# Kernel optimization log

Measured on AMD Instinct MI355X. Metric: run time of the kernel, lower is better.

The kernel has to match this reference:

```python
import jax, jax.numpy as jnp
import numpy as np

N_NODES = 100000
N_EDGES = 1600000
IN_CH = 128
HID = 32
N_GRAPHS = 64


def _gcn_conv(x, src, dst, W, b, n_nodes):
    # PyG GCNConv defaults: x' = D^{-1/2} (A + I) D^{-1/2} (x W) + b
    h = x @ W                                   # [N, out]
    loop = jnp.arange(n_nodes, dtype=src.dtype)
    s = jnp.concatenate([src, loop])            # add self-loops
    d = jnp.concatenate([dst, loop])
    deg = jax.ops.segment_sum(jnp.ones_like(d, dtype=h.dtype), d, num_segments=n_nodes)
    dinv = jnp.where(deg > 0, jax.lax.rsqrt(deg), 0.0)
    norm = dinv[s] * dinv[d]                    # [E+N]
    msg = h[s] * norm[:, None]                  # gather + scale
    out = jax.ops.segment_sum(msg, d, num_segments=n_nodes)  # scatter-add
    return out + b


def setup_inputs() -> dict:
    key = jax.random.key(0)
    ks = jax.random.split(key, 8)
    x = jax.random.normal(ks[0], (N_NODES, IN_CH), dtype=jnp.float32)
    edge_index = jax.random.randint(ks[1], (2, N_EDGES), 0, N_NODES, dtype=jnp.int32)
    batch = jnp.sort(jax.random.randint(ks[2], (N_NODES,), 0, N_GRAPHS, dtype=jnp.int32))
    W1 = jax.random.normal(ks[3], (IN_CH, HID), dtype=jnp.float32) * (1.0 / np.sqrt(IN_CH))
    b1 = jnp.zeros((HID,), dtype=jnp.float32)
    W2 = jax.random.normal(ks[4], (HID, HID), dtype=jnp.float32) * (1.0 / np.sqrt(HID))
    b2 = jnp.zeros((HID,), dtype=jnp.float32)
    Ws = jax.random.normal(ks[5], (HID, HID), dtype=jnp.float32) * (1.0 / np.sqrt(HID))
    bs = jnp.zeros((HID,), dtype=jnp.float32)
    return {"x": x, "edge_index": edge_index, "batch": batch,
            "W1": W1, "b1": b1, "W2": W2, "b2": b2, "Ws": Ws, "bs": bs}


def reference(x, edge_index, batch, W1, b1, W2, b2, Ws, bs):
    src, dst = edge_index[0], edge_index[1]
    n = x.shape[0]
    h = _gcn_conv(x, src, dst, W1, b1, n)
    h = jax.nn.relu(h)
    h = _gcn_conv(h, src, dst, W2, b2, n)       # [N, HID] node embeddings
    # global_mean_pool over graph ids
    ones = jnp.ones((n,), dtype=h.dtype)
    cnt = jax.ops.segment_sum(ones, batch, num_segments=N_GRAPHS)
    gsum = jax.ops.segment_sum(h, batch, num_segments=N_GRAPHS)
    g = gsum / jnp.maximum(cnt, 1.0)[:, None]   # [G, HID]
    summary = g @ Ws + bs
    return summary, h
```

## Files before the change

kernel.cpp:

```cpp
#include <hip/hip_runtime.h>

#define N_NODES  100000
#define N_EDGES  1600000
#define IN_CH    128
#define HID      32
#define N_GRAPHS 64

#define NBIN   391
#define CHUNK  4096
#define MGRID  391
#define STG    5120

#define OFF_B      0
#define OFF_EDGEPK 3200000
#define OFF_CSR    4800000
#define OFF_COLT   6400000
#define OFF_BINB   6400391
#define OFF_ROWPTR 6400784
#define OFF_DINV   6500785

__device__ __forceinline__ unsigned bfr(float f) {
    unsigned u = __float_as_uint(f);
    u += 0x7fffu + ((u >> 16) & 1u);
    return u >> 16;
}
__device__ __forceinline__ float bflo(unsigned w) { return __uint_as_float(w << 16); }
__device__ __forceinline__ float bfhi(unsigned w) { return __uint_as_float(w & 0xffff0000u); }

__global__ __launch_bounds__(512) void hist_kernel(const int* __restrict__ dst,
                                                   int* __restrict__ H) {
    __shared__ int s[512];
    int t = threadIdx.x, wg = blockIdx.x;
    s[t] = 0;
    __syncthreads();
    int e0 = wg * CHUNK, e1 = min(e0 + CHUNK, N_EDGES);
    for (int e = e0 + t; e < e1; e += 512) {
        int d = dst[e];
        if ((unsigned)d < N_NODES) atomicAdd(&s[d >> 8], 1);
    }
    __syncthreads();
    if (t < NBIN) H[t * MGRID + wg] = s[t];
}

__global__ __launch_bounds__(512) void scanrow_kernel(int* __restrict__ H,
                                                      int* __restrict__ colT) {
    __shared__ int s[512];
    int t = threadIdx.x, bin = blockIdx.x;
    s[t] = (t < MGRID) ? H[bin * MGRID + t] : 0;
    __syncthreads();
    for (int off = 1; off < 512; off <<= 1) {
        int v = (t >= off) ? s[t - off] : 0;
        __syncthreads();
        if (t >= off) s[t] += v;
        __syncthreads();
    }
    if (t < MGRID) H[bin * MGRID + t] = t ? s[t - 1] : 0;
    if (t == 0) colT[bin] = s[MGRID - 1];
}

__global__ __launch_bounds__(512) void scanbase_kernel(const int* __restrict__ colT,
                                                       int* __restrict__ binB,
                                                       int* __restrict__ row_ptr) {
    __shared__ int s[512];
    int t = threadIdx.x;
    s[t] = (t < NBIN) ? colT[t] : 0;
    __syncthreads();
    for (int off = 1; off < 512; off <<= 1) {
        int v = (t >= off) ? s[t - off] : 0;
        __syncthreads();
        if (t >= off) s[t] += v;
        __syncthreads();
    }
    if (t < NBIN) binB[t] = t ? s[t - 1] : 0;
    if (t == 0) { binB[NBIN] = s[NBIN - 1]; row_ptr[N_NODES] = s[NBIN - 1]; }
}

__global__ __launch_bounds__(512) void msplit_kernel(const int* __restrict__ src,
                                                     const int* __restrict__ dst,
                                                     const int* __restrict__ H,
                                                     const int* __restrict__ binB,
                                                     int* __restrict__ edgepk) {
    __shared__ int s[512];
    __shared__ int cur[NBIN];
    __shared__ int gb[NBIN];
    __shared__ int stage[CHUNK];
    __shared__ int gof[CHUNK];
    int t = threadIdx.x, wg = blockIdx.x;
    s[t] = 0;
    __syncthreads();
    int e0 = wg * CHUNK, e1 = min(e0 + CHUNK, N_EDGES);
    for (int e = e0 + t; e < e1; e += 512) {
        int d = dst[e];
        if ((unsigned)d < N_NODES) atomicAdd(&s[d >> 8], 1);
    }
    __syncthreads();
    for (int off = 1; off < 512; off <<= 1) {
        int v = (t >= off) ? s[t - off] : 0;
        __syncthreads();
        if (t >= off) s[t] += v;
        __syncthreads();
    }
    if (t < NBIN) {
        int lo = t ? s[t - 1] : 0;
        cur[t] = lo;
        gb[t] = binB[t] + H[t * MGRID + wg] - lo;
    }
    __syncthreads();
    for (int e = e0 + t; e < e1; e += 512) {
        int d = dst[e];
        if ((unsigned)d < N_NODES) {
            int b = d >> 8;
            int p = atomicAdd(&cur[b], 1);
            stage[p] = (src[e] << 8) | (d & 255);
            gof[p] = gb[b];
        }
    }
    __syncthreads();
    int total = s[511];
    for (int p = t; p < total; p += 512)
        edgepk[gof[p] + p] = stage[p];
}

__global__ __launch_bounds__(256) void csr2_kernel(const int* __restrict__ edgepk,
                                                   const int* __restrict__ binB,
                                                   int* __restrict__ row_ptr,
                                                   float* __restrict__ dinv,
                                                   int* __restrict__ csr) {
    __shared__ int cnt[256], s[256], cur[256];
    __shared__ int stage[STG];
    int t = threadIdx.x, bin = blockIdx.x;
    int ebase = binB[bin], eend = binB[bin + 1];
    int n = eend - ebase;
    cnt[t] = 0;
    __syncthreads();
    for (int p = ebase + t; p < eend; p += 256)
        atomicAdd(&cnt[edgepk[p] & 255], 1);
    __syncthreads();
    s[t] = cnt[t];
    __syncthreads();
    for (int off = 1; off < 256; off <<= 1) {
        int v = (t >= off) ? s[t - off] : 0;
        __syncthreads();
        if (t >= off) s[t] += v;
        __syncthreads();
    }
    int excl = t ? s[t - 1] : 0;
    int node = (bin << 8) + t;
    if (node < N_NODES) {
        dinv[node] = rsqrtf((float)(cnt[t] + 1));
        row_ptr[node] = ebase + excl;
    }
    cur[t] = excl;
    __syncthreads();
    for (int p = ebase + t; p < eend; p += 256) {
        int w = edgepk[p];
        int l = atomicAdd(&cur[w & 255], 1);
        int sv = w >> 8;
        if (l < STG) stage[l] = sv;
        else csr[ebase + l] = sv;
    }
    __syncthreads();
    int lim = min(n, STG);
    for (int l = t; l < lim; l += 256)
        csr[ebase + l] = stage[l];
}

#define XS1 132
__global__ __launch_bounds__(256) void gemm1_kernel(const float* __restrict__ x,
                                                    const float* __restrict__ W1,
                                                    const float* __restrict__ dinv,
                                                    unsigned* __restrict__ Bu) {
    __shared__ float Wl[IN_CH * HID];
    __shared__ float xs[32 * XS1];
    int tid = threadIdx.x;
    for (int j = tid; j < IN_CH * HID / 4; j += 256)
        ((float4*)Wl)[j] = ((const float4*)W1)[j];
    int row0 = blockIdx.x * 32;
    const float4* x4 = (const float4*)(x + (size_t)row0 * IN_CH);
    for (int j = tid; j < 32 * IN_CH / 4; j += 256) {
        int r = j >> 5, k4 = j & 31;
        ((float4*)&xs[r * XS1])[k4] = x4[j];
    }
    __syncthreads();
    int r = tid >> 3, cg = (tid & 7) * 4;
    const float* xr = &xs[r * XS1];
    float4 acc = {0.f, 0.f, 0.f, 0.f};
    #pragma unroll 8
    for (int k = 0; k < IN_CH; ++k) {
        float xv = xr[k];
        float4 w = *(const float4*)&Wl[k * HID + cg];
        acc.x += xv * w.x; acc.y += xv * w.y; acc.z += xv * w.z; acc.w += xv * w.w;
    }
    int row = row0 + r;
    float dv = dinv[row];
    uint2 p;
    p.x = bfr(acc.x * dv) | (bfr(acc.y * dv) << 16);
    p.y = bfr(acc.z * dv) | (bfr(acc.w * dv) << 16);
    *(uint2*)&Bu[(size_t)row * 16 + (tid & 7) * 2] = p;
}

#define XS2 36
__global__ __launch_bounds__(256) void gemm2_kernel(const float* __restrict__ in,
                                                    const float* __restrict__ W2,
                                                    const float* __restrict__ dinv,
                                                    unsigned* __restrict__ Bu) {
    __shared__ float Wl[HID * HID];
    __shared__ float xs[32 * XS2];
    int tid = threadIdx.x;
    ((float4*)Wl)[tid] = ((const float4*)W2)[tid];
    int row0 = blockIdx.x * 32;
    const float4* in4 = (const float4*)(in + (size_t)row0 * HID);
    {
        int r = tid >> 3, k4 = tid & 7;
        ((float4*)&xs[r * XS2])[k4] = in4[tid];
    }
    __syncthreads();
    int r = tid >> 3, cg = (tid & 7) * 4;
    const float* xr = &xs[r * XS2];
    float4 acc = {0.f, 0.f, 0.f, 0.f};
    #pragma unroll
    for (int k = 0; k < HID; ++k) {
        float xv = xr[k];
        float4 w = *(const float4*)&Wl[k * HID + cg];
        acc.x += xv * w.x; acc.y += xv * w.y; acc.z += xv * w.z; acc.w += xv * w.w;
    }
    int row = row0 + r;
    float dv = dinv[row];
    uint2 p;
    p.x = bfr(acc.x * dv) | (bfr(acc.y * dv) << 16);
    p.y = bfr(acc.z * dv) | (bfr(acc.w * dv) << 16);
    *(uint2*)&Bu[(size_t)row * 16 + (tid & 7) * 2] = p;
}

__global__ __launch_bounds__(256) void layer_kernel(const unsigned* __restrict__ Bu,
                                                    const int* __restrict__ csr,
                                                    const int* __restrict__ row_ptr,
                                                    const float* __restrict__ dinv,
                                                    const float* __restrict__ bias,
                                                    float* __restrict__ out,
                                                    int relu) {
    int tid = threadIdx.x;
    int node = blockIdx.x * 16 + (tid >> 4);
    int c2 = tid & 15;
    unsigned ws = Bu[(size_t)node * 16 + c2];
    float a0 = bflo(ws), a1 = bfhi(ws);
    int j = row_ptr[node], re = row_ptr[node + 1];
    for (; j + 8 <= re; j += 8) {
        int s0 = csr[j + 0], s1 = csr[j + 1], s2 = csr[j + 2], s3 = csr[j + 3];
        int s4 = csr[j + 4], s5 = csr[j + 5], s6 = csr[j + 6], s7 = csr[j + 7];
        unsigned w0 = Bu[(size_t)s0 * 16 + c2], w1 = Bu[(size_t)s1 * 16 + c2];
        unsigned w2 = Bu[(size_t)s2 * 16 + c2], w3 = Bu[(size_t)s3 * 16 + c2];
        unsigned w4 = Bu[(size_t)s4 * 16 + c2], w5 = Bu[(size_t)s5 * 16 + c2];
        unsigned w6 = Bu[(size_t)s6 * 16 + c2], w7 = Bu[(size_t)s7 * 16 + c2];
        a0 += ((bflo(w0) + bflo(w1)) + (bflo(w2) + bflo(w3)))
            + ((bflo(w4) + bflo(w5)) + (bflo(w6) + bflo(w7)));
        a1 += ((bfhi(w0) + bfhi(w1)) + (bfhi(w2) + bfhi(w3)))
            + ((bfhi(w4) + bfhi(w5)) + (bfhi(w6) + bfhi(w7)));
    }
    if (j + 4 <= re) {
        int s0 = csr[j], s1 = csr[j + 1], s2 = csr[j + 2], s3 = csr[j + 3];
        unsigned w0 = Bu[(size_t)s0 * 16 + c2], w1 = Bu[(size_t)s1 * 16 + c2];
        unsigned w2 = Bu[(size_t)s2 * 16 + c2], w3 = Bu[(size_t)s3 * 16 + c2];
        a0 += (bflo(w0) + bflo(w1)) + (bflo(w2) + bflo(w3));
        a1 += (bfhi(w0) + bfhi(w1)) + (bfhi(w2) + bfhi(w3));
        j += 4;
    }
    for (; j < re; ++j) {
        unsigned w = Bu[(size_t)csr[j] * 16 + c2];
        a0 += bflo(w); a1 += bfhi(w);
    }
    float dv = dinv[node];
    float2 o;
    o.x = a0 * dv + bias[2 * c2];
    o.y = a1 * dv + bias[2 * c2 + 1];
    if (relu) { o.x = fmaxf(o.x, 0.f); o.y = fmaxf(o.y, 0.f); }
    *(float2*)&out[(size_t)node * HID + 2 * c2] = o;
}

__global__ __launch_bounds__(256) void pool_kernel(const float* __restrict__ h,
                                                   const int* __restrict__ batch,
                                                   float* __restrict__ gsum,
                                                   float* __restrict__ cnt) {
    __shared__ float pool[N_GRAPHS * HID];
    __shared__ float cntl[N_GRAPHS];
    __shared__ int gmin, gmax;
    int t = threadIdx.x;
    for (int j = t; j < N_GRAPHS * HID; j += 256) pool[j] = 0.f;
    if (t < N_GRAPHS) cntl[t] = 0.f;
    if (t == 0) { gmin = N_GRAPHS; gmax = -1; }
    __syncthreads();
    int start = blockIdx.x * 256;
    int end = min(start + 256, N_NODES);
    int c = t & 31;
    float racc = 0.f;
    int rg = -1, rcnt = 0;
    for (int nb = start + (t >> 5); nb < end; nb += 8) {
        float v = h[(size_t)nb * HID + c];
        int g = batch[nb];
        if (g != rg) {
            if ((unsigned)rg < N_GRAPHS) {
                atomicAdd(&pool[rg * HID + c], racc);
                if (c == 0) {
                    atomicAdd(&cntl[rg], (float)rcnt);
                    atomicMin(&gmin, rg); atomicMax(&gmax, rg);
                }
            }
            rg = g; racc = v; rcnt = 1;
        } else { racc += v; ++rcnt; }
    }
    if ((unsigned)rg < N_GRAPHS) {
        atomicAdd(&pool[rg * HID + c], racc);
        if (c == 0) {
            atomicAdd(&cntl[rg], (float)rcnt);
            atomicMin(&gmin, rg); atomicMax(&gmax, rg);
        }
    }
    __syncthreads();
    int lo = gmin, hi = gmax;
    if (hi >= lo) {
        int span = (hi - lo + 1) * HID;
        for (int j = t; j < span; j += 256)
            atomicAdd(&gsum[lo * HID + j], pool[lo * HID + j]);
        for (int j = t; j <= hi - lo; j += 256)
            atomicAdd(&cnt[lo + j], cntl[lo + j]);
    }
}

__global__ void summary_kernel(const float* __restrict__ gsum, const float* __restrict__ cnt,
                               const float* __restrict__ Ws, const float* __restrict__ bs,
                               float* __restrict__ out) {
    int g = blockIdx.x, c = threadIdx.x;
    float inv = 1.f / fmaxf(cnt[g], 1.f);
    float acc = bs[c];
    #pragma unroll
    for (int k = 0; k < HID; ++k)
        acc += gsum[g * HID + k] * inv * Ws[k * HID + c];
    out[g * HID + c] = acc;
}

extern "C" void kernel_launch(void* const* d_in, const int* in_sizes, int n_in,
                              void* d_out, int out_size, void* d_ws, size_t ws_size,
                              hipStream_t stream) {
    const float* x    = (const float*)d_in[0];
    const int* edge   = (const int*)d_in[1];
    const int* src    = edge;
    const int* dst    = edge + N_EDGES;
    const int* batch  = (const int*)d_in[2];
    const float* W1   = (const float*)d_in[3];
    const float* b1   = (const float*)d_in[4];
    const float* W2   = (const float*)d_in[5];
    const float* b2   = (const float*)d_in[6];
    const float* Ws   = (const float*)d_in[7];
    const float* bs   = (const float*)d_in[8];

    float* ws      = (float*)d_ws;
    unsigned* Bu   = (unsigned*)(ws + OFF_B);
    int*   H       = (int*)(ws + OFF_B);
    int*   edgepk  = (int*)(ws + OFF_EDGEPK);
    int*   csr     = (int*)(ws + OFF_CSR);
    int*   colT    = (int*)(ws + OFF_COLT);
    int*   binB    = (int*)(ws + OFF_BINB);
    int*   row_ptr = (int*)(ws + OFF_ROWPTR);
    float* dinv    = ws + OFF_DINV;
    float* gsum    = ws + OFF_EDGEPK;
    float* cnt     = gsum + N_GRAPHS * HID;

    float* out     = (float*)d_out;
    float* out_sum = out;
    float* out_h   = out + N_GRAPHS * HID;

    hist_kernel    <<<MGRID, 512, 0, stream>>>(dst, H);
    scanrow_kernel <<<NBIN,  512, 0, stream>>>(H, colT);
    scanbase_kernel<<<1,     512, 0, stream>>>(colT, binB, row_ptr);
    msplit_kernel  <<<MGRID, 512, 0, stream>>>(src, dst, H, binB, edgepk);
    csr2_kernel    <<<NBIN,  256, 0, stream>>>(edgepk, binB, row_ptr, dinv, csr);

    gemm1_kernel<<<N_NODES / 32, 256, 0, stream>>>(x, W1, dinv, Bu);
    layer_kernel<<<N_NODES / 16, 256, 0, stream>>>(Bu, csr, row_ptr, dinv, b1, out_h, 1);

    gemm2_kernel<<<N_NODES / 32, 256, 0, stream>>>(out_h, W2, dinv, Bu);
    layer_kernel<<<N_NODES / 16, 256, 0, stream>>>(Bu, csr, row_ptr, dinv, b2, out_h, 0);

    hipMemsetAsync(gsum, 0, (N_GRAPHS * HID + N_GRAPHS) * sizeof(float), stream);
    pool_kernel<<<NBIN, 256, 0, stream>>>(out_h, batch, gsum, cnt);
    summary_kernel<<<N_GRAPHS, HID, 0, stream>>>(gsum, cnt, Ws, bs, out_sum);
}
```

Baseline: 240.2 us.

## Split neighbor gather into two source-node halves for cache locality

The CSR build now sorts each node's neighbors by whether the source id falls in the lower or upper half of the node range and records a row midpoint. Each aggregation layer then runs as two passes, each gathering only from one half of the feature table, so the working set of random gathers is halved and fits the cache better. The first pass writes partial sums with nontemporal stores and the second reads them back, adds its own half, and applies normalization, bias and ReLU. The cost is an extra kernel launch per layer plus a round trip of the partial sums through memory.

```diff
diff --git a/kernel.cpp b/kernel.cpp
--- a/kernel.cpp
+++ b/kernel.cpp
@@ -5,6 +5,7 @@
 #define IN_CH    128
 #define HID      32
 #define N_GRAPHS 64
+#define HALF     50000
 
 #define NBIN   391
 #define CHUNK  4096
@@ -18,6 +19,9 @@
 #define OFF_BINB   6400391
 #define OFF_ROWPTR 6400784
 #define OFF_DINV   6500785
+#define OFF_RMID   6600785
+
+typedef float v2f __attribute__((ext_vector_type(2)));
 
 __device__ __forceinline__ unsigned bfr(float f) {
     unsigned u = __float_as_uint(f);
@@ -121,47 +125,57 @@
         edgepk[gof[p] + p] = stage[p];
 }
 
-__global__ __launch_bounds__(256) void csr2_kernel(const int* __restrict__ edgepk,
+__global__ __launch_bounds__(512) void csr2_kernel(const int* __restrict__ edgepk,
                                                    const int* __restrict__ binB,
                                                    int* __restrict__ row_ptr,
+                                                   int* __restrict__ row_mid,
                                                    float* __restrict__ dinv,
                                                    int* __restrict__ csr) {
-    __shared__ int cnt[256], s[256], cur[256];
+    __shared__ int cnt[512], s[512], cur[512];
     __shared__ int stage[STG];
     int t = threadIdx.x, bin = blockIdx.x;
     int ebase = binB[bin], eend = binB[bin + 1];
     int n = eend - ebase;
     cnt[t] = 0;
     __syncthreads();
-    for (int p = ebase + t; p < eend; p += 256)
-        atomicAdd(&cnt[edgepk[p] & 255], 1);
+    for (int p = ebase + t; p < eend; p += 512) {
+        int w = edgepk[p];
+        int sv = (int)((unsigned)w >> 8);
+        int key = ((w & 255) << 1) | (sv >= HALF);
+        atomicAdd(&cnt[key], 1);
+    }
     __syncthreads();
     s[t] = cnt[t];
     __syncthreads();
-    for (int off = 1; off < 256; off <<= 1) {
+    for (int off = 1; off < 512; off <<= 1) {
         int v = (t >= off) ? s[t - off] : 0;
         __syncthreads();
         if (t >= off) s[t] += v;
         __syncthreads();
     }
     int excl = t ? s[t - 1] : 0;
-    int node = (bin << 8) + t;
+    int node = (bin << 8) + (t >> 1);
     if (node < N_NODES) {
-        dinv[node] = rsqrtf((float)(cnt[t] + 1));
-        row_ptr[node] = ebase + excl;
+        if ((t & 1) == 0) {
+            row_ptr[node] = ebase + excl;
+            dinv[node] = rsqrtf((float)(cnt[t] + cnt[t + 1] + 1));
+        } else {
+            row_mid[node] = ebase + excl;
+        }
     }
     cur[t] = excl;
     __syncthreads();
-    for (int p = ebase + t; p < eend; p += 256) {
+    for (int p = ebase + t; p < eend; p += 512) {
         int w = edgepk[p];
-        int l = atomicAdd(&cur[w & 255], 1);
-        int sv = w >> 8;
+        int sv = (int)((unsigned)w >> 8);
+        int key = ((w & 255) << 1) | (sv >= HALF);
+        int l = atomicAdd(&cur[key], 1);
         if (l < STG) stage[l] = sv;
         else csr[ebase + l] = sv;
     }
     __syncthreads();
     int lim = min(n, STG);
-    for (int l = t; l < lim; l += 256)
+    for (int l = t; l < lim; l += 512)
         csr[ebase + l] = stage[l];
 }
 
@@ -232,19 +246,29 @@
     *(uint2*)&Bu[(size_t)row * 16 + (tid & 7) * 2] = p;
 }
 
-__global__ __launch_bounds__(256) void layer_kernel(const unsigned* __restrict__ Bu,
-                                                    const int* __restrict__ csr,
-                                                    const int* __restrict__ row_ptr,
-                                                    const float* __restrict__ dinv,
-                                                    const float* __restrict__ bias,
-                                                    float* __restrict__ out,
-                                                    int relu) {
+__global__ __launch_bounds__(256) void gather_half_kernel(const unsigned* __restrict__ Bu,
+                                                          const int* __restrict__ csr,
+                                                          const int* __restrict__ jlo,
+                                                          const int* __restrict__ jhi,
+                                                          const float* __restrict__ dinv,
+                                                          const float* __restrict__ bias,
+                                                          float* __restrict__ out,
+                                                          int pass, int relu) {
     int tid = threadIdx.x;
     int node = blockIdx.x * 16 + (tid >> 4);
     int c2 = tid & 15;
-    unsigned ws = Bu[(size_t)node * 16 + c2];
-    float a0 = bflo(ws), a1 = bfhi(ws);
-    int j = row_ptr[node], re = row_ptr[node + 1];
+    float p0 = 0.f, p1 = 0.f;
+    if (pass) {
+        v2f pv = __builtin_nontemporal_load((const v2f*)&out[(size_t)node * HID + 2 * c2]);
+        p0 = pv.x; p1 = pv.y;
+    }
+    float a0 = 0.f, a1 = 0.f;
+    int addself = pass ? (node >= HALF) : (node < HALF);
+    if (addself) {
+        unsigned ws0 = Bu[(size_t)node * 16 + c2];
+        a0 = bflo(ws0); a1 = bfhi(ws0);
+    }
+    int j = jlo[node], re = jhi[node];
     for (; j + 8 <= re; j += 8) {
         int s0 = csr[j + 0], s1 = csr[j + 1], s2 = csr[j + 2], s3 = csr[j + 3];
         int s4 = csr[j + 4], s5 = csr[j + 5], s6 = csr[j + 6], s7 = csr[j + 7];
@@ -269,12 +293,18 @@
         unsigned w = Bu[(size_t)csr[j] * 16 + c2];
         a0 += bflo(w); a1 += bfhi(w);
     }
-    float dv = dinv[node];
-    float2 o;
-    o.x = a0 * dv + bias[2 * c2];
-    o.y = a1 * dv + bias[2 * c2 + 1];
-    if (relu) { o.x = fmaxf(o.x, 0.f); o.y = fmaxf(o.y, 0.f); }
-    *(float2*)&out[(size_t)node * HID + 2 * c2] = o;
+    v2f o;
+    if (!pass) {
+        o.x = a0; o.y = a1;
+        __builtin_nontemporal_store(o, (v2f*)&out[(size_t)node * HID + 2 * c2]);
+    } else {
+        a0 += p0; a1 += p1;
+        float dv = dinv[node];
+        o.x = a0 * dv + bias[2 * c2];
+        o.y = a1 * dv + bias[2 * c2 + 1];
+        if (relu) { o.x = fmaxf(o.x, 0.f); o.y = fmaxf(o.y, 0.f); }
+        *(v2f*)&out[(size_t)node * HID + 2 * c2] = o;
+    }
 }
 
 __global__ __launch_bounds__(256) void pool_kernel(const float* __restrict__ h,
@@ -362,6 +392,7 @@
     int*   binB    = (int*)(ws + OFF_BINB);
     int*   row_ptr = (int*)(ws + OFF_ROWPTR);
     float* dinv    = ws + OFF_DINV;
+    int*   row_mid = (int*)(ws + OFF_RMID);
     float* gsum    = ws + OFF_EDGEPK;
     float* cnt     = gsum + N_GRAPHS * HID;
 
@@ -373,13 +404,19 @@
     scanrow_kernel <<<NBIN,  512, 0, stream>>>(H, colT);
     scanbase_kernel<<<1,     512, 0, stream>>>(colT, binB, row_ptr);
     msplit_kernel  <<<MGRID, 512, 0, stream>>>(src, dst, H, binB, edgepk);
-    csr2_kernel    <<<NBIN,  256, 0, stream>>>(edgepk, binB, row_ptr, dinv, csr);
+    csr2_kernel    <<<NBIN,  512, 0, stream>>>(edgepk, binB, row_ptr, row_mid, dinv, csr);
 
     gemm1_kernel<<<N_NODES / 32, 256, 0, stream>>>(x, W1, dinv, Bu);
-    layer_kernel<<<N_NODES / 16, 256, 0, stream>>>(Bu, csr, row_ptr, dinv, b1, out_h, 1);
+    gather_half_kernel<<<N_NODES / 16, 256, 0, stream>>>(Bu, csr, row_ptr, row_mid,
+                                                         dinv, b1, out_h, 0, 0);
+    gather_half_kernel<<<N_NODES / 16, 256, 0, stream>>>(Bu, csr, row_mid, row_ptr + 1,
+                                                         dinv, b1, out_h, 1, 1);
 
     gemm2_kernel<<<N_NODES / 32, 256, 0, stream>>>(out_h, W2, dinv, Bu);
-    layer_kernel<<<N_NODES / 16, 256, 0, stream>>>(Bu, csr, row_ptr, dinv, b2, out_h, 0);
+    gather_half_kernel<<<N_NODES / 16, 256, 0, stream>>>(Bu, csr, row_ptr, row_mid,
+                                                         dinv, b2, out_h, 0, 0);
+    gather_half_kernel<<<N_NODES / 16, 256, 0, stream>>>(Bu, csr, row_mid, row_ptr + 1,
+                                                         dinv, b2, out_h, 1, 0);
 
     hipMemsetAsync(gsum, 0, (N_GRAPHS * HID + N_GRAPHS) * sizeof(float), stream);
     pool_kernel<<<NBIN, 256, 0, stream>>>(out_h, batch, gsum, cnt);
```

After: 261.0 us. +8.6%, slower.
